# Kernel tuning notes

Measured on AMD Instinct MI355X. Metric: run time of the kernel, lower is better.

Reference implementation:

```python
import jax, jax.numpy as jnp
import numpy as np

N = 50000   # nodes
E = 800000  # edges
D = 256     # in = hidden = out channels
R = 16      # num_relations (last index reserved for self-loops)
B = 8       # num_bases
LN_EPS = 1e-5


def setup_inputs() -> dict:
    key = jax.random.key(0)
    ks = jax.random.split(key, 20)
    s_basis = np.sqrt(2.0 / (D + D)).astype(np.float32)  # glorot-ish scale
    s_att = np.sqrt(2.0 / (R + B)).astype(np.float32)
    inp = {
        "x": jax.random.normal(ks[0], (N, D), dtype=jnp.float32),
        "edge_index": jax.random.randint(ks[1], (2, E), 0, N),
        "edge_type": jax.random.randint(ks[2], (E,), 0, R),
        "edge_attr": jax.random.uniform(ks[3], (E,), dtype=jnp.float32),
        # layer 1 params
        "basis1": jax.random.normal(ks[4], (B, D, D), dtype=jnp.float32) * s_basis,
        "att1": jax.random.normal(ks[5], (R, B), dtype=jnp.float32) * s_att,
        "root1": jax.random.normal(ks[6], (D, D), dtype=jnp.float32) * s_basis,
        "bias1": jnp.zeros((D,), dtype=jnp.float32),
        "ln1_g": jnp.ones((D,), dtype=jnp.float32),
        "ln1_b": jnp.zeros((D,), dtype=jnp.float32),
        # layer 2 params
        "basis2": jax.random.normal(ks[7], (B, D, D), dtype=jnp.float32) * s_basis,
        "att2": jax.random.normal(ks[8], (R, B), dtype=jnp.float32) * s_att,
        "root2": jax.random.normal(ks[9], (D, D), dtype=jnp.float32) * s_basis,
        "bias2": jnp.zeros((D,), dtype=jnp.float32),
        "ln2_g": jnp.ones((D,), dtype=jnp.float32),
        "ln2_b": jnp.zeros((D,), dtype=jnp.float32),
    }
    return inp


def _layer_norm(x, g, b):
    mu = jnp.mean(x, axis=-1, keepdims=True)
    var = jnp.mean(jnp.square(x - mu), axis=-1, keepdims=True)
    return (x - mu) * jax.lax.rsqrt(var + LN_EPS) * g + b


def _rgcn_layer(x, edge_index, edge_type, edge_attr, basis, att, root, bias):
    n = x.shape[0]
    r = att.shape[0]
    # W_r = sum_b a_rb V_b ; then per-relation transform of every node.
    weight = jnp.einsum('rb,bio->rio', att, basis)          # [R, D, D]
    H = jnp.einsum('ni,rio->nro', x, weight)                # [N, R, D]
    # append self-loops with relation index R-1 and confidence 1.0
    loop = jnp.arange(n, dtype=edge_index.dtype)
    src = jnp.concatenate([edge_index[0], loop])
    dst = jnp.concatenate([edge_index[1], loop])
    et = jnp.concatenate([edge_type, jnp.full((n,), r - 1, dtype=edge_type.dtype)])
    ea = jnp.concatenate([edge_attr, jnp.ones((n,), dtype=x.dtype)])
    msg = H[src, et] * ea[:, None]                          # [E+N, D]
    summ = jax.ops.segment_sum(msg, dst, num_segments=n)
    cnt = jax.ops.segment_sum(jnp.ones_like(ea), dst, num_segments=n)
    agg = summ / cnt[:, None]                               # scatter-mean (cnt >= 1 via self-loops)
    return agg + x @ root + bias


def reference(x, edge_index, edge_type, edge_attr,
              basis1, att1, root1, bias1, ln1_g, ln1_b,
              basis2, att2, root2, bias2, ln2_g, ln2_b):
    # input_proj / output_proj are Identity since in == hidden == out.
    h = x
    h_out = _rgcn_layer(h, edge_index, edge_type, edge_attr, basis1, att1, root1, bias1)
    h = jax.nn.relu(_layer_norm(h + h_out, ln1_g, ln1_b))
    h_out = _rgcn_layer(h, edge_index, edge_type, edge_attr, basis2, att2, root2, bias2)
    h = jax.nn.relu(_layer_norm(h + h_out, ln2_g, ln2_b))
    return h
```

## Files before the change

### kernel.cpp

```cpp
#include <hip/hip_runtime.h>
#include <stdint.h>

#define D 256
#define RREL 16
#define BB 8
#define K9 2304
#define LN_EPS 1e-5f
#define NT (K9 / 64)
#define BUFB 49152

typedef __attribute__((ext_vector_type(8))) short frag8;
typedef __attribute__((ext_vector_type(4))) float floatx4;
typedef __attribute__((ext_vector_type(2))) float float2v;

__device__ __forceinline__ unsigned short f2bf(float f) {
    union { float f; uint32_t u; } v; v.f = f;
    uint32_t r = (v.u + 0x7FFFu + ((v.u >> 16) & 1u)) >> 16;
    return (unsigned short)r;
}
__device__ __forceinline__ float bf2f(unsigned short u) {
    union { uint32_t u; float f; } v; v.u = (uint32_t)u << 16;
    return v.f;
}
__device__ __forceinline__ float2v bfpair(uint32_t d) {
    union { uint32_t u; float f; } lo, hi;
    lo.u = d << 16; hi.u = d & 0xFFFF0000u;
    return (float2v){lo.f, hi.f};
}

__device__ __forceinline__ float2v pk_mul(float2v a, float2v b) {
    float2v d;
    asm("v_pk_mul_f32 %0, %1, %2" : "=v"(d) : "v"(a), "v"(b));
    return d;
}
__device__ __forceinline__ void pk_fma_lo(float2v& acc, float2v c, float2v x) {
    asm("v_pk_fma_f32 %0, %1, %2, %0 op_sel:[0,0,0] op_sel_hi:[1,0,1]"
        : "+v"(acc) : "v"(c), "v"(x));
}
__device__ __forceinline__ void pk_fma_hi(float2v& acc, float2v c, float2v x) {
    asm("v_pk_fma_f32 %0, %1, %2, %0 op_sel:[0,1,0] op_sel_hi:[1,1,1]"
        : "+v"(acc) : "v"(c), "v"(x));
}

__device__ __forceinline__ void gl2lds16(const unsigned short* g, char* l) {
    __builtin_amdgcn_global_load_lds((const __attribute__((address_space(1))) void*)g,
                                     (__attribute__((address_space(3))) void*)l, 16, 0, 0);
}

__global__ __launch_bounds__(256) void k_cvt(const float* __restrict__ src,
                                             unsigned short* __restrict__ dst, int n4) {
    int i = blockIdx.x * 256 + threadIdx.x;
    if (i >= n4) return;
    float4 v = ((const float4*)src)[i];
    ushort4 o = make_ushort4(f2bf(v.x), f2bf(v.y), f2bf(v.z), f2bf(v.w));
    ((ushort4*)dst)[i] = o;
}

__global__ __launch_bounds__(256) void k_deg(const int* __restrict__ ei,
                                             int* __restrict__ deg, int E) {
    int t = blockIdx.x * 256 + threadIdx.x;
    int stride = gridDim.x * 256;
    int d[4];
#pragma unroll
    for (int j = 0; j < 4; ++j) {
        int e = t + j * stride;
        d[j] = (e < E) ? ei[E + e] : -1;
    }
#pragma unroll
    for (int j = 0; j < 4; ++j)
        if (d[j] >= 0) atomicAdd(&deg[d[j]], 1);
}

__global__ __launch_bounds__(256) void k_scan1(const int* __restrict__ deg,
                                               int* __restrict__ csum, int N) {
    __shared__ int sh[256];
    int n = blockIdx.x * 256 + threadIdx.x;
    sh[threadIdx.x] = (n < N) ? deg[n] : 0;
    __syncthreads();
    for (int off = 128; off > 0; off >>= 1) {
        if (threadIdx.x < off) sh[threadIdx.x] += sh[threadIdx.x + off];
        __syncthreads();
    }
    if (threadIdx.x == 0) csum[blockIdx.x] = sh[0];
}

__global__ __launch_bounds__(256) void k_scan2(int* __restrict__ csum, int nch,
                                               int* __restrict__ rowptr, int N) {
    __shared__ int sh[256];
    int tid = threadIdx.x;
    if (nch <= 256) {
        int v = (tid < nch) ? csum[tid] : 0;
        sh[tid] = v;
        __syncthreads();
        for (int off = 1; off < 256; off <<= 1) {
            int t = (tid >= off) ? sh[tid - off] : 0;
            __syncthreads();
            sh[tid] += t;
            __syncthreads();
        }
        if (tid < nch) csum[tid] = sh[tid] - v;
        if (tid == 255) rowptr[N] = sh[255];
    } else if (tid == 0) {
        int s = 0;
        for (int i = 0; i < nch; ++i) { int c = csum[i]; csum[i] = s; s += c; }
        rowptr[N] = s;
    }
}

__global__ __launch_bounds__(256) void k_scan3(const int* __restrict__ deg,
                                               const int* __restrict__ csum,
                                               int* __restrict__ rowptr,
                                               int* __restrict__ cursor,
                                               float* __restrict__ cnt, int N) {
    __shared__ int sh[256];
    int tid = threadIdx.x;
    int n = blockIdx.x * 256 + tid;
    int v = (n < N) ? deg[n] : 0;
    sh[tid] = v;
    __syncthreads();
    for (int off = 1; off < 256; off <<= 1) {
        int t = (tid >= off) ? sh[tid - off] : 0;
        __syncthreads();
        sh[tid] += t;
        __syncthreads();
    }
    int excl = sh[tid] - v + csum[blockIdx.x];
    if (n < N) {
        rowptr[n] = excl;
        cursor[n] = excl;
        cnt[n] = (float)(v + 1);
    }
}

__global__ __launch_bounds__(256) void k_scatter(const int* __restrict__ ei,
                                                 const int* __restrict__ et,
                                                 const float* __restrict__ ea,
                                                 int* __restrict__ cursor,
                                                 int2* __restrict__ ep, int E) {
    int t = blockIdx.x * 256 + threadIdx.x;
    int stride = gridDim.x * 256;
    int src[4], dst[4], typ[4]; float w[4]; bool v[4];
#pragma unroll
    for (int j = 0; j < 4; ++j) {
        int e = t + j * stride;
        v[j] = (e < E);
        if (v[j]) { src[j] = ei[e]; dst[j] = ei[E + e]; typ[j] = et[e]; w[j] = ea[e]; }
    }
    int p[4];
#pragma unroll
    for (int j = 0; j < 4; ++j)
        if (v[j]) p[j] = atomicAdd(&cursor[dst[j]], 1);
#pragma unroll
    for (int j = 0; j < 4; ++j)
        if (v[j]) ep[p[j]] = make_int2(src[j] | (typ[j] << 24), __float_as_int(w[j]));
}

__global__ __launch_bounds__(256) void k_prep_w(const float* __restrict__ basis,
                                                const float* __restrict__ root,
                                                unsigned short* __restrict__ Wt) {
    __shared__ float tile[64][65];
    int k0 = blockIdx.x * 64, o0 = blockIdx.y * 64;
    const float* src = (k0 < BB * D) ? (basis + (size_t)k0 * D)
                                     : (root + (size_t)(k0 - BB * D) * D);
    int tid = threadIdx.x;
#pragma unroll
    for (int t = 0; t < 16; ++t) {
        int idx = t * 256 + tid;
        int kk = idx >> 6, oo = idx & 63;
        tile[kk][oo] = src[(size_t)kk * D + o0 + oo];
    }
    __syncthreads();
#pragma unroll
    for (int t = 0; t < 16; ++t) {
        int idx = t * 256 + tid;
        int oo = idx >> 6, kk = idx & 63;
        Wt[(size_t)(o0 + oo) * K9 + k0 + kk] = f2bf(tile[kk][oo]);
    }
}

__device__ __forceinline__ void edge_fma(float2v g2[4][4], float2v c0, float2v c1,
                                         float2v c2, float2v c3,
                                         float2v x0, float2v x1) {
    pk_fma_lo(g2[0][0], c0, x0); pk_fma_lo(g2[1][0], c1, x0);
    pk_fma_lo(g2[2][0], c2, x0); pk_fma_lo(g2[3][0], c3, x0);
    pk_fma_hi(g2[0][1], c0, x0); pk_fma_hi(g2[1][1], c1, x0);
    pk_fma_hi(g2[2][1], c2, x0); pk_fma_hi(g2[3][1], c3, x0);
    pk_fma_lo(g2[0][2], c0, x1); pk_fma_lo(g2[1][2], c1, x1);
    pk_fma_lo(g2[2][2], c2, x1); pk_fma_lo(g2[3][2], c3, x1);
    pk_fma_hi(g2[0][3], c0, x1); pk_fma_hi(g2[1][3], c1, x1);
    pk_fma_hi(g2[2][3], c2, x1); pk_fma_hi(g2[3][3], c3, x1);
}

__device__ __forceinline__ void do_edge(float2v g2[4][4], const float* att_s,
                                        int2 pe, uint2 ud) {
    int r = (unsigned)pe.x >> 24;
    const float4* Ar = (const float4*)&att_s[r * BB];
    float4 a0 = Ar[0], a1 = Ar[1];
    float we = __int_as_float(pe.y);
    float2v w2 = {we, we};
    float2v c0 = pk_mul(w2, (float2v){a0.x, a0.y});
    float2v c1 = pk_mul(w2, (float2v){a0.z, a0.w});
    float2v c2 = pk_mul(w2, (float2v){a1.x, a1.y});
    float2v c3 = pk_mul(w2, (float2v){a1.z, a1.w});
    float2v x0 = bfpair(ud.x), x1 = bfpair(ud.y);
    edge_fma(g2, c0, c1, c2, c3, x0, x1);
}

__global__ __launch_bounds__(256) void k_gather(
    const unsigned short* __restrict__ xb, const float* __restrict__ att,
    const int* __restrict__ rowptr, const int2* __restrict__ ep,
    const float* __restrict__ cnt, unsigned short* __restrict__ G,
    int n0, int rows, int N) {
    __shared__ __align__(32) float att_s[RREL * BB];
    int tid = threadIdx.x;
    if (tid < RREL * BB) att_s[tid] = att[tid];
    __syncthreads();
    int wv = tid >> 6, lane = tid & 63;
    int rloc = blockIdx.x * 4 + wv;
    if (rloc >= rows) return;
    int n = n0 + rloc;
    unsigned short* gout = G + (size_t)rloc * K9 + lane * 4;
    if (n >= N) {
        ushort4 z = make_ushort4(0, 0, 0, 0);
#pragma unroll
        for (int b = 0; b <= BB; ++b) *(ushort4*)(gout + b * D) = z;
        return;
    }
    uint2 xu = *(const uint2*)&xb[(size_t)n * D + lane * 4];
    float2v xs0 = bfpair(xu.x), xs1 = bfpair(xu.y);
    float xv[4] = {xs0.x, xs0.y, xs1.x, xs1.y};

    float2v g2[4][4];
#pragma unroll
    for (int bp = 0; bp < 4; ++bp) {
        float2v ap = {att_s[(RREL - 1) * BB + 2 * bp],
                      att_s[(RREL - 1) * BB + 2 * bp + 1]};
#pragma unroll
        for (int j = 0; j < 4; ++j) {
            float2v xs = {xv[j], xv[j]};
            g2[bp][j] = ap * xs;
        }
    }

    int e0 = rowptr[n], e1 = rowptr[n + 1];
    int e = e0;
    for (; e + 4 <= e1; e += 4) {
        int2 pa = ep[e], pb = ep[e + 1], pc = ep[e + 2], pd = ep[e + 3];
        uint2 uA = *(const uint2*)&xb[(size_t)(pa.x & 0xFFFFFF) * D + lane * 4];
        uint2 uB = *(const uint2*)&xb[(size_t)(pb.x & 0xFFFFFF) * D + lane * 4];
        uint2 uC = *(const uint2*)&xb[(size_t)(pc.x & 0xFFFFFF) * D + lane * 4];
        uint2 uD = *(const uint2*)&xb[(size_t)(pd.x & 0xFFFFFF) * D + lane * 4];
        do_edge(g2, att_s, pa, uA);
        do_edge(g2, att_s, pb, uB);
        do_edge(g2, att_s, pc, uC);
        do_edge(g2, att_s, pd, uD);
    }
    if (e + 2 <= e1) {
        int2 pa = ep[e], pb = ep[e + 1];
        uint2 uA = *(const uint2*)&xb[(size_t)(pa.x & 0xFFFFFF) * D + lane * 4];
        uint2 uB = *(const uint2*)&xb[(size_t)(pb.x & 0xFFFFFF) * D + lane * 4];
        do_edge(g2, att_s, pa, uA);
        do_edge(g2, att_s, pb, uB);
        e += 2;
    }
    if (e < e1) {
        int2 pa = ep[e];
        uint2 uA = *(const uint2*)&xb[(size_t)(pa.x & 0xFFFFFF) * D + lane * 4];
        do_edge(g2, att_s, pa, uA);
    }
#pragma unroll
    for (int bp = 0; bp < 4; ++bp) {
        ushort4 o0 = make_ushort4(f2bf(g2[bp][0].x), f2bf(g2[bp][1].x),
                                  f2bf(g2[bp][2].x), f2bf(g2[bp][3].x));
        *(ushort4*)(gout + (2 * bp) * D) = o0;
        ushort4 o1 = make_ushort4(f2bf(g2[bp][0].y), f2bf(g2[bp][1].y),
                                  f2bf(g2[bp][2].y), f2bf(g2[bp][3].y));
        *(ushort4*)(gout + (2 * bp + 1) * D) = o1;
    }
    float cn = cnt[n];
    ushort4 o = make_ushort4(f2bf(cn * xv[0]), f2bf(cn * xv[1]),
                             f2bf(cn * xv[2]), f2bf(cn * xv[3]));
    *(ushort4*)(gout + BB * D) = o;
}

__global__ __launch_bounds__(1024, 4) void k_gemm(
    const unsigned short* __restrict__ G, const unsigned short* __restrict__ Wt,
    const float* __restrict__ hin, const float* __restrict__ cnt,
    const float* __restrict__ bias, const float* __restrict__ gln,
    const float* __restrict__ bln, float* __restrict__ hout,
    unsigned short* __restrict__ houtb, int n0, int N) {
    __shared__ __align__(16) char smem[2 * BUFB];
    float* ps   = (float*)smem;
    float* pq   = ps + 512;
    float* mu_s = ps + 1024;
    float* rs_s = ps + 1152;

    int tid = threadIdx.x;
    int wv = tid >> 6, lane = tid & 63;
    int quad = lane >> 4, l16 = lane & 15;
    int wm = wv >> 2, wn = wv & 3;
    int grow = blockIdx.x * 128;
    int nb = n0 + grow;

    int arow_s = tid >> 3, aslot_s = tid & 7;
    const unsigned short* gA =
        G + (size_t)(grow + arow_s) * K9 + ((aslot_s ^ (arow_s & 7)) << 3);
    char* lA = smem + (tid << 4);
    const unsigned short* gB[2]; char* lB[2];
#pragma unroll
    for (int t = 0; t < 2; ++t) {
        int c = t * 1024 + tid;
        int brow = c >> 3, bslot = c & 7;
        gB[t] = Wt + (size_t)brow * K9 + ((bslot ^ (brow & 7)) << 3);
        lB[t] = smem + 16384 + (c << 4);
    }

    floatx4 acc[2][4];
#pragma unroll
    for (int mf = 0; mf < 2; ++mf)
#pragma unroll
        for (int nf = 0; nf < 4; ++nf) acc[mf][nf] = (floatx4){0.f, 0.f, 0.f, 0.f};

    auto STAGE = [&](int it, int soff) {
        int koff = it * 64;
        gl2lds16(gA + koff, lA + soff);
        gl2lds16(gB[0] + koff, lB[0] + soff);
        gl2lds16(gB[1] + koff, lB[1] + soff);
    };
    auto COMPUTE = [&](int soff) {
        const char* Ab = smem + soff;
        const char* Bb = Ab + 16384;
#pragma unroll
        for (int kc = 0; kc < 2; ++kc) {
            int g = kc * 4 + quad;
            frag8 a[2], b[4];
#pragma unroll
            for (int mf = 0; mf < 2; ++mf) {
                int arow = wm * 32 + mf * 16 + l16;
                a[mf] = *(const frag8*)(Ab + arow * 128 + ((g ^ (arow & 7)) << 4));
            }
#pragma unroll
            for (int nf = 0; nf < 4; ++nf) {
                int brow = wn * 64 + nf * 16 + l16;
                b[nf] = *(const frag8*)(Bb + brow * 128 + ((g ^ (brow & 7)) << 4));
            }
#pragma unroll
            for (int mf = 0; mf < 2; ++mf)
#pragma unroll
                for (int nf = 0; nf < 4; ++nf)
                    acc[mf][nf] = __builtin_amdgcn_mfma_f32_16x16x32_bf16(
                        a[mf], b[nf], acc[mf][nf], 0, 0, 0);
        }
    };

    STAGE(0, 0);
    __syncthreads();
    for (int it = 0; it < NT; it += 2) {
        STAGE(it + 1, BUFB);
        COMPUTE(0);
        __syncthreads();
        if (it + 2 < NT) STAGE(it + 2, 0);
        COMPUTE(BUFB);
        __syncthreads();
    }

    int col[4]; float bic[4];
#pragma unroll
    for (int nf = 0; nf < 4; ++nf) {
        col[nf] = wn * 64 + nf * 16 + l16;
        bic[nf] = bias[col[nf]];
    }
#pragma unroll
    for (int mf = 0; mf < 2; ++mf) {
#pragma unroll
        for (int r = 0; r < 4; ++r) {
            int row = wm * 32 + mf * 16 + quad * 4 + r;
            int n = nb + row;
            float s = 0.f, sq = 0.f;
            if (n < N) {
                float inv = 1.0f / cnt[n];
                const float* hp = hin + (size_t)n * D;
#pragma unroll
                for (int nf = 0; nf < 4; ++nf) {
                    float v = acc[mf][nf][r] * inv + hp[col[nf]] + bic[nf];
                    acc[mf][nf][r] = v;
                    s += v; sq += v * v;
                }
            }
            s += __shfl_xor(s, 1); sq += __shfl_xor(sq, 1);
            s += __shfl_xor(s, 2); sq += __shfl_xor(sq, 2);
            s += __shfl_xor(s, 4); sq += __shfl_xor(sq, 4);
            s += __shfl_xor(s, 8); sq += __shfl_xor(sq, 8);
            if (l16 == 0) {
                ps[row * 4 + wn] = s;
                pq[row * 4 + wn] = sq;
            }
        }
    }
    __syncthreads();
    if (tid < 128) {
        float s  = ps[tid * 4] + ps[tid * 4 + 1] + ps[tid * 4 + 2] + ps[tid * 4 + 3];
        float sq = pq[tid * 4] + pq[tid * 4 + 1] + pq[tid * 4 + 2] + pq[tid * 4 + 3];
        float mu = s * (1.f / D);
        mu_s[tid] = mu;
        rs_s[tid] = rsqrtf(sq * (1.f / D) - mu * mu + LN_EPS);
    }
    __syncthreads();

    float gc[4], bc[4];
#pragma unroll
    for (int nf = 0; nf < 4; ++nf) {
        gc[nf] = gln[col[nf]];
        bc[nf] = bln[col[nf]];
    }
#pragma unroll
    for (int mf = 0; mf < 2; ++mf) {
#pragma unroll
        for (int r = 0; r < 4; ++r) {
            int row = wm * 32 + mf * 16 + quad * 4 + r;
            int n = nb + row;
            if (n >= N) continue;
            float mu = mu_s[row], rs = rs_s[row];
            float* op = hout + (size_t)n * D;
#pragma unroll
            for (int nf = 0; nf < 4; ++nf) {
                float o = fmaxf((acc[mf][nf][r] - mu) * rs * gc[nf] + bc[nf], 0.f);
                op[col[nf]] = o;
                if (houtb) houtb[(size_t)n * D + col[nf]] = f2bf(o);
            }
        }
    }
}

extern "C" void kernel_launch(void* const* d_in, const int* in_sizes, int n_in,
                              void* d_out, int out_size, void* d_ws, size_t ws_size,
                              hipStream_t stream) {
    const float* x      = (const float*)d_in[0];
    const int*   ei     = (const int*)d_in[1];
    const int*   et     = (const int*)d_in[2];
    const float* ea     = (const float*)d_in[3];
    const float* basis1 = (const float*)d_in[4];
    const float* att1   = (const float*)d_in[5];
    const float* root1  = (const float*)d_in[6];
    const float* bias1  = (const float*)d_in[7];
    const float* g1     = (const float*)d_in[8];
    const float* b1     = (const float*)d_in[9];
    const float* basis2 = (const float*)d_in[10];
    const float* att2   = (const float*)d_in[11];
    const float* root2  = (const float*)d_in[12];
    const float* bias2  = (const float*)d_in[13];
    const float* g2     = (const float*)d_in[14];
    const float* b2     = (const float*)d_in[15];
    float* out = (float*)d_out;

    int N = in_sizes[0] / D;
    int E = in_sizes[2];
    int nch = (N + 255) / 256;
    int Mp = ((N + 63) / 64) * 64;
    int T = Mp / 64;
    int Tpad = (T + 1) & ~1;

    char* p = (char*)d_ws;
    size_t used = 0;
    auto alloc = [&](size_t bytes) {
        char* q = p;
        size_t a = (bytes + 255) & ~(size_t)255;
        p += a; used += a;
        return q;
    };
    float*          h1     = (float*)alloc((size_t)N * D * 4);
    unsigned short* xb     = (unsigned short*)alloc((size_t)N * D * 2);
    unsigned short* h1b    = (unsigned short*)alloc((size_t)N * D * 2);
    unsigned short* Wt     = (unsigned short*)alloc((size_t)K9 * D * 2);
    int*            deg    = (int*)alloc((size_t)N * 4);
    int*            rowptr = (int*)alloc((size_t)(N + 1) * 4);
    int*            cursor = (int*)alloc((size_t)N * 4);
    float*          cnt    = (float*)alloc((size_t)N * 4);
    int2*           ep     = (int2*)alloc((size_t)E * 8);
    int*            csum   = (int*)alloc((size_t)nch * 4);
    size_t remain = (ws_size > used + 256) ? (ws_size - used - 256) : 0;
    size_t tile_bytes = (size_t)64 * K9 * 2;
    int ct_max = (int)(remain / tile_bytes);
    if (ct_max < 2) ct_max = 2;
    if (ct_max > Tpad) ct_max = Tpad;
    unsigned short* G = (unsigned short*)alloc((size_t)ct_max * tile_bytes);

    int nch2 = (Tpad + ct_max - 1) / ct_max;
    int ct = (Tpad + nch2 - 1) / nch2;
    ct = (ct + 1) & ~1;
    if (ct > ct_max) ct = ct_max & ~1;
    if (ct < 2) ct = 2;

    hipMemsetAsync(deg, 0, (size_t)N * 4, stream);
    int gE4 = (E + 1023) / 1024;
    k_deg<<<gE4, 256, 0, stream>>>(ei, deg, E);
    k_scan1<<<nch, 256, 0, stream>>>(deg, csum, N);
    k_scan2<<<1, 256, 0, stream>>>(csum, nch, rowptr, N);
    k_scan3<<<nch, 256, 0, stream>>>(deg, csum, rowptr, cursor, cnt, N);
    k_scatter<<<gE4, 256, 0, stream>>>(ei, et, ea, cursor, ep, E);
    k_cvt<<<(N * D / 4 + 255) / 256, 256, 0, stream>>>(x, xb, N * D / 4);

    const float* bas[2]  = {basis1, basis2};
    const float* attp[2] = {att1, att2};
    const float* rt[2]   = {root1, root2};
    const float* bi[2]   = {bias1, bias2};
    const float* lg[2]   = {g1, g2};
    const float* lb[2]   = {b1, b2};
    const unsigned short* gin[2] = {xb, h1b};
    const float* hres[2] = {x, h1};
    float*          hof[2] = {h1, out};
    unsigned short* hob[2] = {h1b, nullptr};

    for (int L = 0; L < 2; ++L) {
        k_prep_w<<<dim3(K9 / 64, D / 64), 256, 0, stream>>>(bas[L], rt[L], Wt);
        for (int c0 = 0; c0 < Tpad; c0 += ct) {
            int tiles = (Tpad - c0 < ct) ? (Tpad - c0) : ct;
            int rows = tiles * 64;
            int n0 = c0 * 64;
            k_gather<<<rows / 4, 256, 0, stream>>>(gin[L], attp[L], rowptr, ep,
                                                   cnt, G, n0, rows, N);
            k_gemm<<<rows / 128, 1024, 0, stream>>>(G, Wt, hres[L], cnt, bi[L],
                                                    lg[L], lb[L], hof[L], hob[L],
                                                    n0, N);
        }
    }
}
```

Measured before the change: 628.5 us.

## Triple-buffer GEMM LDS stages with partial vmcnt waits

The GEMM main loop moves from double buffering to a three-stage LDS ring, prefetching two tiles ahead. It waits with explicit s_waitcnt vmcnt counts so older loads can complete while newer ones stay in flight, instead of draining fully at each __syncthreads. Shared memory grows to 3x48KB and the occupancy hint in launch_bounds is dropped. The cost is fewer resident blocks per CU, and the hard-coded vmcnt values assume a fixed number of loads per STAGE.

```diff
diff --git a/kernel.cpp b/kernel.cpp
--- a/kernel.cpp
+++ b/kernel.cpp
@@ -283,13 +283,13 @@
     *(ushort4*)(gout + BB * D) = o;
 }
 
-__global__ __launch_bounds__(1024, 4) void k_gemm(
+__global__ __launch_bounds__(1024) void k_gemm(
     const unsigned short* __restrict__ G, const unsigned short* __restrict__ Wt,
     const float* __restrict__ hin, const float* __restrict__ cnt,
     const float* __restrict__ bias, const float* __restrict__ gln,
     const float* __restrict__ bln, float* __restrict__ hout,
     unsigned short* __restrict__ houtb, int n0, int N) {
-    __shared__ __align__(16) char smem[2 * BUFB];
+    __shared__ __align__(16) char smem[3 * BUFB];
     float* ps   = (float*)smem;
     float* pq   = ps + 512;
     float* mu_s = ps + 1024;
@@ -354,15 +354,29 @@
     };
 
     STAGE(0, 0);
-    __syncthreads();
-    for (int it = 0; it < NT; it += 2) {
-        STAGE(it + 1, BUFB);
-        COMPUTE(0);
-        __syncthreads();
-        if (it + 2 < NT) STAGE(it + 2, 0);
-        COMPUTE(BUFB);
-        __syncthreads();
-    }
+    STAGE(1, BUFB);
+    int it = 0;
+    for (; it + 2 < NT; ++it) {
+        int sc = (it % 3) * BUFB;
+        int sp = ((it + 2) % 3) * BUFB;
+        STAGE(it + 2, sp);
+        asm volatile("s_waitcnt vmcnt(6)" ::: "memory");
+        __builtin_amdgcn_s_barrier();
+        __builtin_amdgcn_sched_barrier(0);
+        COMPUTE(sc);
+        __builtin_amdgcn_s_barrier();
+        __builtin_amdgcn_sched_barrier(0);
+    }
+    asm volatile("s_waitcnt vmcnt(3)" ::: "memory");
+    __builtin_amdgcn_s_barrier();
+    __builtin_amdgcn_sched_barrier(0);
+    COMPUTE((it % 3) * BUFB);
+    ++it;
+    asm volatile("s_waitcnt vmcnt(0)" ::: "memory");
+    __builtin_amdgcn_s_barrier();
+    __builtin_amdgcn_sched_barrier(0);
+    COMPUTE((it % 3) * BUFB);
+    __syncthreads();
 
     int col[4]; float bic[4];
 #pragma unroll
```

After: 622.8 us. About the same (-0.9%).
